# Kernel tuning notes

Hardware: AMD Instinct MI355X
Metric: run time of the kernel (lower is better)

Reference implementation:

```python
import jax, jax.numpy as jnp
import numpy as np

NEG = -1e30  # finite stand-in for -inf so logsumexp grads stay finite


def ctc_loss_mean(y_true, log_probs_tm, input_length, label_length, blank=0):
    """CTC loss (forward algorithm in log space), mean over batch.

    log_probs_tm: [T, B, C] time-major log-probabilities.
    y_true:       [B, L] dense int labels (blank=0 excluded from real labels).
    """
    T, B, C = log_probs_tm.shape
    L = y_true.shape[1]
    S = 2 * L + 1  # extended label length: blank, l1, blank, l2, ...
    ll = jnp.clip(label_length, 1, L)
    il = jnp.clip(input_length, 1, T)

    # Extended label sequence: blanks at even positions, labels at odd.
    ext = jnp.full((B, S), blank, dtype=jnp.int32).at[:, 1::2].set(y_true.astype(jnp.int32))
    ext_m2 = jnp.concatenate([jnp.full((B, 2), -1, jnp.int32), ext[:, :-2]], axis=1)
    # Skip transition (s-2 -> s) allowed only for label positions with no repeat.
    allow_skip = ((jnp.arange(S) % 2 == 1)[None, :]) & (ext != ext_m2)

    lp0 = jnp.take_along_axis(log_probs_tm[0], ext, axis=1)  # [B, S]
    alpha0 = jnp.full((B, S), NEG, log_probs_tm.dtype)
    alpha0 = alpha0.at[:, 0].set(lp0[:, 0]).at[:, 1].set(lp0[:, 1])

    def step(alpha, xs):
        lp_t, t = xs
        lpe = jnp.take_along_axis(lp_t, ext, axis=1)  # [B, S]
        a1 = jnp.concatenate([jnp.full((B, 1), NEG, alpha.dtype), alpha[:, :-1]], axis=1)
        a2 = jnp.concatenate([jnp.full((B, 2), NEG, alpha.dtype), alpha[:, :-2]], axis=1)
        a2 = jnp.where(allow_skip, a2, NEG)
        new = jax.nn.logsumexp(jnp.stack([alpha, a1, a2]), axis=0) + lpe
        # Freeze alpha once past each example's input_length.
        return jnp.where((t < il)[:, None], new, alpha), None

    alpha, _ = jax.lax.scan(step, alpha0, (log_probs_tm[1:], jnp.arange(1, T)))

    # Loss = -log(alpha[2*ll-1] + alpha[2*ll]) at the final (frozen) time step.
    idx = jnp.stack([2 * ll - 1, 2 * ll], axis=1)  # [B, 2]
    end_vals = jnp.take_along_axis(alpha, idx, axis=1)
    loss = -jax.nn.logsumexp(end_vals, axis=1)
    return jnp.mean(loss)


def setup_inputs() -> dict:
    key = jax.random.key(0)
    kx, kl, ki, kj = jax.random.split(key, 4)
    B, T, C, L = 64, 1024, 128, 256
    # y_pred are probabilities (module applies log), so softmax random logits.
    y_pred = jax.nn.softmax(jax.random.normal(kx, (B, T, C), jnp.float32), axis=-1)
    y_true = jax.random.randint(kl, (B, L), 1, C, jnp.int32)  # blank=0 excluded
    input_length = jax.random.randint(ki, (B,), T // 2, T + 1, jnp.int32)
    label_length = jax.random.randint(kj, (B,), L // 2, L + 1, jnp.int32)
    return {"y_true": y_true, "y_pred": y_pred,
            "input_length": input_length, "label_length": label_length}


def reference(y_true, y_pred, input_length, label_length):
    # Mirror CTCLayer.call: log + transpose to time-major, reshape lengths.
    log_tm = jnp.log(jnp.transpose(y_pred, (1, 0, 2)))  # [T, B, C]
    loss = ctc_loss_mean(y_true, log_tm,
                         input_length.reshape(-1), label_length.reshape(-1),
                         blank=0)
    return log_tm, loss
```

## Files before the change

kernel.cpp:

```cpp
#include <hip/hip_runtime.h>
#include <math.h>

constexpr int B = 64;
constexpr int T = 1024;
constexpr int C = 128;
constexpr int L = 256;
constexpr int S = 2 * L + 1;
constexpr int TRB = 2048;
constexpr int N4 = T * B * C / 4;

template <int N> struct IC { static constexpr int value = N; };

__device__ __forceinline__ float shr1(float x) {
    return __int_as_float(__builtin_amdgcn_update_dpp(
        0, __float_as_int(x), 0x138 , 0xf, 0xf, false));
}

__global__ __launch_bounds__(64, 1) void ctc_fused(
    const float* __restrict__ yp,
    const int*   __restrict__ yt,
    const int*   __restrict__ il_,
    const int*   __restrict__ ll_,
    float* __restrict__ out_log,
    float* __restrict__ out_loss)
{
    if (blockIdx.x >= B) {
        int gid = (blockIdx.x - B) * 64 + threadIdx.x;
        const float4* in4 = (const float4*)yp;
        float4* o4 = (float4*)out_log;
        for (int i = gid; i < N4; i += TRB * 64) {
            int c4 = i & 31;
            int tb = i >> 5;
            int bb = tb & 63;
            int tt = tb >> 6;
            float4 v = in4[(bb * T + tt) * 32 + c4];
            float4 r;
            r.x = __logf(v.x); r.y = __logf(v.y);
            r.z = __logf(v.z); r.w = __logf(v.w);
            o4[i] = r;
        }
        return;
    }

    const int b    = blockIdx.x;
    const int lane = threadIdx.x;

    __shared__ float lsh[2048];
    __shared__ float afin[S];

    int il = il_[b]; il = min(max(il, 1), T);
    int ll = ll_[b]; ll = min(max(ll, 1), L);
    const float* yb = yp + (size_t)b * T * C;

    int4 y4  = *(const int4*)(yt + b * L + 4 * lane);
    int  po  = lane ? 4 * lane - 4 : 0;
    int4 py4 = *(const int4*)(yt + b * L + po);
    int  ppw = yt[b * L + (lane >= 2 ? 4 * lane - 5 : 0)];

    int lab[8]   = {py4.x, py4.y, py4.z, py4.w, y4.x, y4.y, y4.z, y4.w};
    int labm1[8] = {ppw,   py4.x, py4.y, py4.z, py4.w, y4.x, y4.y, y4.z};
    float skf[8];
    #pragma unroll
    for (int k = 0; k < 8; ++k)
        skf[k] = ((4 * lane + k >= 5) && (lab[k] != labm1[k])) ? 1.f : 0.f;

    const int c0 = y4.x, c1 = y4.y, c2 = y4.z, c3 = y4.w;

    auto ldpair = [&](int m) -> float4 {
        int r = 2 * m + 1 + (lane >> 5);
        r = r > T - 1 ? T - 1 : r;
        return ((const float4*)(yb + (size_t)r * C))[lane & 31];
    };

    float p00 = yb[0];
    float p0l = yb[c0];

    float4 q0 = ldpair(0), q1 = ldpair(1);
    float4 q2 = ldpair(2), q3 = ldpair(3);
    float4 prr[8];
    #pragma unroll
    for (int m = 4; m <= 11; ++m) prr[m & 7] = ldpair(m);

    ((float4*)(lsh +   0))[lane] = q0;
    ((float4*)(lsh + 256))[lane] = q1;
    ((float4*)(lsh + 512))[lane] = q2;
    ((float4*)(lsh + 768))[lane] = q3;

    float gv[4][4][4], gbv[4][4];
    #pragma unroll
    for (int q = 0; q < 2; ++q)
        #pragma unroll
        for (int j = 0; j < 4; ++j) {
            const float* base = lsh + q * 512 + j * 128;
            gbv[q][j] = base[0];
            gv[q][j][0] = base[c0]; gv[q][j][1] = base[c1];
            gv[q][j][2] = base[c2]; gv[q][j][3] = base[c3];
        }

    float w[17];
    #pragma unroll
    for (int i = 0; i < 17; ++i) w[i] = 0.f;
    if (lane == 0) { w[8] = p00; w[9] = p0l; }

    auto halo = [&]() {
        #pragma unroll
        for (int k = 0; k < 8; ++k) w[k] = shr1(w[8 + k]);
    };
    halo();

    float ls = 0.f;
    float m_meas = 1.0f;
    int t0 = 0;

    auto group = [&](auto Pc, auto S0c) {
        constexpr int P  = decltype(Pc)::value;
        constexpr int S0 = decltype(S0c)::value;
        constexpr int BF = (P + 2) & 3;
        float g1[4], g2[4], g3[4];
        #pragma unroll
        for (int j = 0; j < 4; ++j) {
            g1[j] = shr1(gv[P][j][1]);
            g2[j] = shr1(gv[P][j][2]);
            g3[j] = shr1(gv[P][j][3]);
        }
        #pragma unroll
        for (int j = 0; j < 4; ++j) {
            #pragma unroll
            for (int i = 16; i >= 2 * (j + 1); --i) {
                float acc = w[i] + w[i - 1];
                float g;
                if (i & 1) {
                    const int k = (i - 1) >> 1;
                    acc = fmaf(skf[k], w[i - 2], acc);
                    g = (k >= 4) ? gv[P][j][k - 4]
                                 : (k == 1 ? g1[j] : (k == 2 ? g2[j] : g3[j]));
                } else {
                    g = gbv[P][j];
                }
                w[i] = acc * g;
            }
        }
        ((float4*)(lsh + BF * 512      ))[lane] = prr[S0];
        ((float4*)(lsh + BF * 512 + 256))[lane] = prr[S0 + 1];
        prr[S0]     = ldpair((t0 >> 1) + 12);
        prr[S0 + 1] = ldpair((t0 >> 1) + 13);
        #pragma unroll
        for (int j = 0; j < 4; ++j) {
            const float* base = lsh + BF * 512 + j * 128;
            gbv[BF][j] = base[0];
            gv[BF][j][0] = base[c0]; gv[BF][j][1] = base[c1];
            gv[BF][j][2] = base[c2]; gv[BF][j][3] = base[c3];
        }
        halo();
        t0 += 4;
    };

    auto rescale = [&](float mm) {
        int eb = (__float_as_int(mm) >> 23) & 0xff;
        int sh = 350 - eb;
        sh = sh > 254 ? 254 : (sh < 1 ? 1 : sh);
        float inv = __int_as_float(sh << 23);
        #pragma unroll
        for (int i = 8; i < 17; ++i) w[i] *= inv;
        ls -= (float)(sh - 127);
    };
    auto maxw = [&]() {
        return fmaxf(fmaxf(fmaxf(w[8], w[9]), fmaxf(w[10], w[11])),
                     fmaxf(fmaxf(w[12], w[13]),
                           fmaxf(fmaxf(w[14], w[15]), w[16])));
    };

    const int full_end = ((il - 1) >> 2) << 2;

    while (t0 + 16 <= full_end) {
        float mm = m_meas;
        mm = fmaxf(mm, __shfl_xor(mm, 1));
        mm = fmaxf(mm, __shfl_xor(mm, 2));
        mm = fmaxf(mm, __shfl_xor(mm, 4));
        group(IC<0>{}, IC<4>{});
        mm = fmaxf(mm, __shfl_xor(mm, 8));
        mm = fmaxf(mm, __shfl_xor(mm, 16));
        mm = fmaxf(mm, __shfl_xor(mm, 32));
        group(IC<1>{}, IC<6>{});
        rescale(mm);
        m_meas = maxw();

        float m2 = m_meas;
        m2 = fmaxf(m2, __shfl_xor(m2, 1));
        m2 = fmaxf(m2, __shfl_xor(m2, 2));
        m2 = fmaxf(m2, __shfl_xor(m2, 4));
        group(IC<2>{}, IC<0>{});
        m2 = fmaxf(m2, __shfl_xor(m2, 8));
        m2 = fmaxf(m2, __shfl_xor(m2, 16));
        m2 = fmaxf(m2, __shfl_xor(m2, 32));
        group(IC<3>{}, IC<2>{});
        rescale(m2);
        m_meas = maxw();
    }

    auto fresh_rescale = [&]() {
        float mm = maxw();
        #pragma unroll
        for (int off = 1; off < 64; off <<= 1) mm = fmaxf(mm, __shfl_xor(mm, off));
        rescale(mm);
    };
    if (t0 + 4 <= full_end) { group(IC<0>{}, IC<4>{}); fresh_rescale(); }
    if (t0 + 4 <= full_end) { group(IC<1>{}, IC<6>{}); fresh_rescale(); }
    if (t0 + 4 <= full_end) { group(IC<2>{}, IC<0>{}); }

    const int ph = (full_end >> 2) & 3;
    float tg[3][4], tb[3];
    switch (ph) {
    case 0:
        #pragma unroll
        for (int j = 0; j < 3; ++j) { tb[j]=gbv[0][j]; tg[j][0]=gv[0][j][0]; tg[j][1]=gv[0][j][1]; tg[j][2]=gv[0][j][2]; tg[j][3]=gv[0][j][3]; }
        break;
    case 1:
        #pragma unroll
        for (int j = 0; j < 3; ++j) { tb[j]=gbv[1][j]; tg[j][0]=gv[1][j][0]; tg[j][1]=gv[1][j][1]; tg[j][2]=gv[1][j][2]; tg[j][3]=gv[1][j][3]; }
        break;
    case 2:
        #pragma unroll
        for (int j = 0; j < 3; ++j) { tb[j]=gbv[2][j]; tg[j][0]=gv[2][j][0]; tg[j][1]=gv[2][j][1]; tg[j][2]=gv[2][j][2]; tg[j][3]=gv[2][j][3]; }
        break;
    default:
        #pragma unroll
        for (int j = 0; j < 3; ++j) { tb[j]=gbv[3][j]; tg[j][0]=gv[3][j][0]; tg[j][1]=gv[3][j][1]; tg[j][2]=gv[3][j][2]; tg[j][3]=gv[3][j][3]; }
        break;
    }
    #pragma unroll
    for (int j = 0; j < 3; ++j) {
        int r = full_end + 1 + j;
        if (r < il) {
            float hh = shr1(w[15]);
            float gb = tb[j];
            float n8  = (w[8] + hh) * gb;
            float n9  = fmaf(skf[4], hh,    w[9]  + w[8])  * tg[j][0];
            float n10 = (w[10] + w[9])  * gb;
            float n11 = fmaf(skf[5], w[9],  w[11] + w[10]) * tg[j][1];
            float n12 = (w[12] + w[11]) * gb;
            float n13 = fmaf(skf[6], w[11], w[13] + w[12]) * tg[j][2];
            float n14 = (w[14] + w[13]) * gb;
            float n15 = fmaf(skf[7], w[13], w[15] + w[14]) * tg[j][3];
            float n16 = (w[16] + w[15]) * gb;
            w[8] = n8;  w[9] = n9;  w[10] = n10; w[11] = n11; w[12] = n12;
            w[13] = n13; w[14] = n14; w[15] = n15; w[16] = n16;
        }
    }

    #pragma unroll
    for (int k = 0; k < 8; ++k) afin[8 * lane + k] = w[8 + k];
    if (lane == 63) afin[512] = w[16];
    __syncthreads();
    if (lane == 0) {
        float e1 = afin[2 * ll - 1];
        float e2 = afin[2 * ll];
        float sum = fmaxf(e1 + e2, 1e-37f);
        float loss = -(__log2f(sum) + ls) * 0.6931471805599453f;
        atomicAdd(out_loss, loss * (1.0f / (float)B));
    }
}

extern "C" void kernel_launch(void* const* d_in, const int* in_sizes, int n_in,
                              void* d_out, int out_size, void* d_ws, size_t ws_size,
                              hipStream_t stream) {
    const int*   y_true = (const int*)d_in[0];
    const float* y_pred = (const float*)d_in[1];
    const int*   in_len = (const int*)d_in[2];
    const int*   lb_len = (const int*)d_in[3];

    float* out_log  = (float*)d_out;
    float* out_loss = (float*)d_out + (size_t)T * B * C;

    hipMemsetAsync(out_loss, 0, sizeof(float), stream);
    ctc_fused<<<B + TRB, 64, 0, stream>>>(y_pred, y_true, in_len, lb_len,
                                          out_log, out_loss);
}
```

Baseline: 197.9 us.

## Use DPP wave max for rescale and restructure log-transpose block tiling

The per-rescale max reduction now uses DPP row shifts/broadcasts plus readlane instead of interleaved shfl_xor chains, and it measures the fresh maximum at rescale time instead of the one-group-stale value. The scale accumulator becomes an integer. The log/transpose blocks now each handle a contiguous 32-timestep chunk of one batch row with a fixed unrolled loop, so reads are contiguous, in place of the earlier grid-stride loop. The aim is to shorten the serial dependency chain in the recurrence, but the reduction now sits directly on the critical path instead of overlapping with the group computation.

```diff
diff --git a/kernel.cpp b/kernel.cpp
--- a/kernel.cpp
+++ b/kernel.cpp
@@ -7,13 +7,29 @@
 constexpr int L = 256;
 constexpr int S = 2 * L + 1;
 constexpr int TRB = 2048;
-constexpr int N4 = T * B * C / 4;
 
 template <int N> struct IC { static constexpr int value = N; };
 
 __device__ __forceinline__ float shr1(float x) {
     return __int_as_float(__builtin_amdgcn_update_dpp(
         0, __float_as_int(x), 0x138 , 0xf, 0xf, false));
+}
+
+template <int CTRL>
+__device__ __forceinline__ float maxdpp(float x) {
+    float t = __int_as_float(__builtin_amdgcn_update_dpp(
+        __float_as_int(x), __float_as_int(x), CTRL, 0xf, 0xf, false));
+    return fmaxf(x, t);
+}
+
+__device__ __forceinline__ float wave_max_dpp(float x) {
+    x = maxdpp<0x111>(x);
+    x = maxdpp<0x112>(x);
+    x = maxdpp<0x114>(x);
+    x = maxdpp<0x118>(x);
+    x = maxdpp<0x142>(x);
+    x = maxdpp<0x143>(x);
+    return __int_as_float(__builtin_amdgcn_readlane(__float_as_int(x), 63));
 }
 
 __global__ __launch_bounds__(64, 1) void ctc_fused(
@@ -24,26 +40,28 @@
     float* __restrict__ out_log,
     float* __restrict__ out_loss)
 {
+    const int lane = threadIdx.x;
     if (blockIdx.x >= B) {
-        int gid = (blockIdx.x - B) * 64 + threadIdx.x;
-        const float4* in4 = (const float4*)yp;
+        int id = blockIdx.x - B;
+        int bb = id >> 5;
+        int ck = id & 31;
+        const float4* src = (const float4*)yp + ((size_t)bb * T + ck * 32) * 32;
         float4* o4 = (float4*)out_log;
-        for (int i = gid; i < N4; i += TRB * 64) {
-            int c4 = i & 31;
-            int tb = i >> 5;
-            int bb = tb & 63;
-            int tt = tb >> 6;
-            float4 v = in4[(bb * T + tt) * 32 + c4];
+        #pragma unroll
+        for (int k = 0; k < 16; ++k) {
+            int o = k * 64 + lane;
+            float4 v = src[o];
+            int tt = ck * 32 + (o >> 5);
+            int c4 = o & 31;
             float4 r;
             r.x = __logf(v.x); r.y = __logf(v.y);
             r.z = __logf(v.z); r.w = __logf(v.w);
-            o4[i] = r;
+            o4[((size_t)tt * B + bb) * 32 + c4] = r;
         }
         return;
     }
 
-    const int b    = blockIdx.x;
-    const int lane = threadIdx.x;
+    const int b = blockIdx.x;
 
     __shared__ float lsh[2048];
     __shared__ float afin[S];
@@ -108,8 +126,7 @@
     };
     halo();
 
-    float ls = 0.f;
-    float m_meas = 1.0f;
+    int lsi = 0;
     int t0 = 0;
 
     auto group = [&](auto Pc, auto S0c) {
@@ -155,57 +172,35 @@
         t0 += 4;
     };
 
-    auto rescale = [&](float mm) {
+    auto maxw = [&]() {
+        return fmaxf(fmaxf(fmaxf(w[8], w[9]), fmaxf(w[10], w[11])),
+                     fmaxf(fmaxf(w[12], w[13]),
+                           fmaxf(fmaxf(w[14], w[15]), w[16])));
+    };
+    auto rescale = [&]() {
+        float mm = wave_max_dpp(maxw());
         int eb = (__float_as_int(mm) >> 23) & 0xff;
         int sh = 350 - eb;
         sh = sh > 254 ? 254 : (sh < 1 ? 1 : sh);
         float inv = __int_as_float(sh << 23);
         #pragma unroll
         for (int i = 8; i < 17; ++i) w[i] *= inv;
-        ls -= (float)(sh - 127);
-    };
-    auto maxw = [&]() {
-        return fmaxf(fmaxf(fmaxf(w[8], w[9]), fmaxf(w[10], w[11])),
-                     fmaxf(fmaxf(w[12], w[13]),
-                           fmaxf(fmaxf(w[14], w[15]), w[16])));
+        lsi -= sh - 127;
     };
 
     const int full_end = ((il - 1) >> 2) << 2;
 
     while (t0 + 16 <= full_end) {
-        float mm = m_meas;
-        mm = fmaxf(mm, __shfl_xor(mm, 1));
-        mm = fmaxf(mm, __shfl_xor(mm, 2));
-        mm = fmaxf(mm, __shfl_xor(mm, 4));
         group(IC<0>{}, IC<4>{});
-        mm = fmaxf(mm, __shfl_xor(mm, 8));
-        mm = fmaxf(mm, __shfl_xor(mm, 16));
-        mm = fmaxf(mm, __shfl_xor(mm, 32));
         group(IC<1>{}, IC<6>{});
-        rescale(mm);
-        m_meas = maxw();
-
-        float m2 = m_meas;
-        m2 = fmaxf(m2, __shfl_xor(m2, 1));
-        m2 = fmaxf(m2, __shfl_xor(m2, 2));
-        m2 = fmaxf(m2, __shfl_xor(m2, 4));
+        rescale();
         group(IC<2>{}, IC<0>{});
-        m2 = fmaxf(m2, __shfl_xor(m2, 8));
-        m2 = fmaxf(m2, __shfl_xor(m2, 16));
-        m2 = fmaxf(m2, __shfl_xor(m2, 32));
         group(IC<3>{}, IC<2>{});
-        rescale(m2);
-        m_meas = maxw();
-    }
-
-    auto fresh_rescale = [&]() {
-        float mm = maxw();
-        #pragma unroll
-        for (int off = 1; off < 64; off <<= 1) mm = fmaxf(mm, __shfl_xor(mm, off));
-        rescale(mm);
-    };
-    if (t0 + 4 <= full_end) { group(IC<0>{}, IC<4>{}); fresh_rescale(); }
-    if (t0 + 4 <= full_end) { group(IC<1>{}, IC<6>{}); fresh_rescale(); }
+        rescale();
+    }
+
+    if (t0 + 4 <= full_end) { group(IC<0>{}, IC<4>{}); rescale(); }
+    if (t0 + 4 <= full_end) { group(IC<1>{}, IC<6>{}); rescale(); }
     if (t0 + 4 <= full_end) { group(IC<2>{}, IC<0>{}); }
 
     const int ph = (full_end >> 2) & 3;
@@ -256,7 +251,7 @@
         float e1 = afin[2 * ll - 1];
         float e2 = afin[2 * ll];
         float sum = fmaxf(e1 + e2, 1e-37f);
-        float loss = -(__log2f(sum) + ls) * 0.6931471805599453f;
+        float loss = -(__log2f(sum) + (float)lsi) * 0.6931471805599453f;
         atomicAdd(out_loss, loss * (1.0f / (float)B));
     }
 }
```

New measurement: 187.0 us. 5.5% less time.
